# Kernel tuning notes

Measured on AMD Instinct MI355X. Metric: run time of the kernel, lower is better.

## Reference

```python
import jax, jax.numpy as jnp
import numpy as np

TEMP = 0.07
BATCH, DIM, NUM_ATTRS = 8192, 512, 4
NUM_PROTOS = 2 ** NUM_ATTRS  # all binary combos present => unique() size is static


def setup_inputs() -> dict:
    key = jax.random.key(0)
    z_flowed = jax.random.normal(key, (BATCH, DIM), dtype=jnp.float32)
    # binary attribute combos, all 16 present; first column = MSB (matches torch.unique row sort)
    combo = jnp.arange(BATCH, dtype=jnp.int32) % NUM_PROTOS
    shifts = jnp.arange(NUM_ATTRS - 1, -1, -1, dtype=jnp.int32)
    attributes = ((combo[:, None] >> shifts[None, :]) & 1).astype(jnp.float32)
    return {"z_flowed": z_flowed, "attributes": attributes}


def _l2norm(x, axis=-1, eps=1e-12):
    n = jnp.sqrt(jnp.sum(x * x, axis=axis, keepdims=True))
    return x / jnp.maximum(n, eps)  # F.normalize semantics


def reference(z_flowed, attributes):
    B, D = z_flowed.shape
    num_attrs = attributes.shape[1]
    P = 2 ** num_attrs
    z_norm = _l2norm(z_flowed, axis=1)

    # inverse indices of torch.unique(attributes, dim=0): binary row -> code (MSB = col 0)
    shifts = jnp.arange(num_attrs - 1, -1, -1)
    inverse = jnp.sum((attributes > 0.5).astype(jnp.int32) * (1 << shifts)[None, :], axis=1)

    # prototype = normalized segment-mean of z_norm per attribute combo (detached)
    sums = jax.ops.segment_sum(z_norm, inverse, num_segments=P)          # [P, D]
    counts = jax.ops.segment_sum(jnp.ones((B,), z_norm.dtype), inverse, num_segments=P)
    means = sums / jnp.maximum(counts, 1.0)[:, None]
    prototypes = jax.lax.stop_gradient(_l2norm(means, axis=1))
    prototypes = jnp.where(counts[:, None] > 0, prototypes, 0.0)

    # prototype contrastive term
    proto_sim = (z_norm @ prototypes.T) / TEMP                            # [B, P]
    exp_sim = jnp.exp(proto_sim)
    pos = exp_sim[jnp.arange(B), inverse]
    alls = jnp.maximum(jnp.sum(exp_sim, axis=1), 1e-8)
    loss = -jnp.mean(jnp.log(pos / alls + 1e-8))

    # pairwise term (positives only when BOTH attribute rows are all-ones)
    pairwise = (z_norm @ z_norm.T) / TEMP                                 # [B, B]
    attr_sim = attributes @ attributes.T
    pos_mask = (attr_sim == num_attrs).astype(z_norm.dtype)
    pos_mask = pos_mask * (1.0 - jnp.eye(B, dtype=z_norm.dtype))
    exp_pw = jnp.exp(pairwise)
    pos_sims = jnp.sum(exp_pw * pos_mask, axis=1)
    all_sims = jnp.sum(exp_pw, axis=1) - jnp.diagonal(exp_pw)
    valid = jnp.sum(pos_mask, axis=1) > 0
    per_row = -jnp.log(pos_sims / (all_sims + 1e-8) + 1e-8)
    n_valid = jnp.sum(valid.astype(z_norm.dtype))
    pairwise_loss = jnp.sum(jnp.where(valid, per_row, 0.0)) / jnp.maximum(n_valid, 1.0)
    loss = jnp.where(n_valid > 0, 0.7 * loss + 0.3 * pairwise_loss, loss)
    return loss
```

## Files before the change

kernel.cpp:

```cpp
#include <hip/hip_runtime.h>
#include <math.h>

#define NB 8192
#define ND 512
#define NPROTO 16
#define NBLK 256
#define TINV 14.285714285714286f
#define PW_BLOCKS 256
#define PL_BLOCKS 256

typedef short short8 __attribute__((ext_vector_type(8)));
typedef float float4v __attribute__((ext_vector_type(4)));

__device__ __forceinline__ unsigned short f2bf(float f) {
  unsigned u = __builtin_bit_cast(unsigned, f);
  unsigned r = (u + 0x7FFFu + ((u >> 16) & 1u)) >> 16;
  return (unsigned short)r;
}
__device__ __forceinline__ float bflo(unsigned u) {
  return __builtin_bit_cast(float, u << 16);
}
__device__ __forceinline__ float bfhi(unsigned u) {
  return __builtin_bit_cast(float, u & 0xFFFF0000u);
}

__global__ __launch_bounds__(512) void k_norm(
    const float* __restrict__ z, const float* __restrict__ attr,
    unsigned short* __restrict__ znb, float* __restrict__ partialSum,
    int* __restrict__ code)
{
  __shared__ float acc[NPROTO * ND];
  const int t = threadIdx.x, lane = t & 63, wid = t >> 6;
  for (int i = t; i < NPROTO * ND; i += 512) acc[i] = 0.f;
  __syncthreads();
  #pragma unroll
  for (int rr = 0; rr < 4; ++rr) {
    const int r = blockIdx.x * 32 + wid * 4 + rr;
    const float4* zr4 = (const float4*)(z + (size_t)r * ND);
    const float4 va = zr4[lane];
    const float4 vb = zr4[lane + 64];
    float v[8] = {va.x, va.y, va.z, va.w, vb.x, vb.y, vb.z, vb.w};
    float s = 0.f;
    #pragma unroll
    for (int k = 0; k < 8; ++k) s += v[k] * v[k];
    #pragma unroll
    for (int o = 32; o > 0; o >>= 1) s += __shfl_xor(s, o);
    const float inv = 1.f / fmaxf(sqrtf(s), 1e-12f);
    const float* a = attr + (size_t)r * 4;
    const int c = (a[0] > 0.5f ? 8 : 0) | (a[1] > 0.5f ? 4 : 0) |
                  (a[2] > 0.5f ? 2 : 0) | (a[3] > 0.5f ? 1 : 0);
    float* accRow = acc + c * ND;
    #pragma unroll
    for (int k = 0; k < 8; ++k) {
      const float zv = v[k] * inv;
      atomicAdd(&accRow[k * 64 + lane], zv);
      znb[(size_t)r * ND + k * 64 + lane] = f2bf(zv);
    }
    if (lane == 0) code[r] = c;
  }
  __syncthreads();
  for (int i = t; i < NPROTO * ND; i += 512) {
    const int p = i >> 9, d = i & 511;
    partialSum[(size_t)((p << 8) | blockIdx.x) * ND + d] = acc[i];
  }
}

__global__ __launch_bounds__(256) void k_reduce1(
    const float* __restrict__ partialSum, float* __restrict__ partial2)
{
  const int t = threadIdx.x;
  const int p = blockIdx.x >> 4, c = blockIdx.x & 15;
  const float* base = partialSum + (size_t)(p * NBLK + c * 16) * ND;
  float s0 = 0.f, s1 = 0.f;
  #pragma unroll
  for (int k = 0; k < 16; ++k) {
    s0 += base[k * ND + t];
    s1 += base[k * ND + t + 256];
  }
  partial2[(size_t)(p * 16 + c) * ND + t] = s0;
  partial2[(size_t)(p * 16 + c) * ND + t + 256] = s1;
}

__global__ __launch_bounds__(512) void k_protonorm(
    const float* __restrict__ partial2, const int* __restrict__ code,
    float* __restrict__ protos, int* __restrict__ validList,
    int* __restrict__ validCnt)
{
  __shared__ float red[8];
  __shared__ int lcnt;
  const int t = threadIdx.x, lane = t & 63, wid = t >> 6;
  const int p = blockIdx.x;
  if (t == 0) lcnt = 0;
  __syncthreads();
  const float* base = partial2 + (size_t)p * 16 * ND;
  float s = 0.f;
  #pragma unroll
  for (int c = 0; c < 16; ++c)
    s += base[c * ND + t];
  float cl = 0.f;
  for (int r = t; r < NB; r += 512) {
    const int match = (code[r] == p) ? 1 : 0;
    cl += (float)match;
    if (p == NPROTO - 1 && match) {
      const int slot = atomicAdd(&lcnt, 1);
      validList[slot] = r;
    }
  }
  #pragma unroll
  for (int o = 32; o > 0; o >>= 1) cl += __shfl_xor(cl, o);
  if (lane == 0) red[wid] = cl;
  __syncthreads();
  const float cTot = red[0]+red[1]+red[2]+red[3]+red[4]+red[5]+red[6]+red[7];
  __syncthreads();
  const float mean = s / fmaxf(cTot, 1.f);
  float sq = mean * mean;
  #pragma unroll
  for (int o = 32; o > 0; o >>= 1) sq += __shfl_xor(sq, o);
  if (lane == 0) red[wid] = sq;
  __syncthreads();
  const float sum = red[0]+red[1]+red[2]+red[3]+red[4]+red[5]+red[6]+red[7];
  const float scale = (cTot > 0.f) ? 1.f / fmaxf(sqrtf(sum), 1e-12f) : 0.f;
  protos[p * ND + t] = mean * scale;
  if (p == NPROTO - 1 && t == 0) validCnt[0] = lcnt;
}

#define PLD (ND + 4)
#define SMEM_BYTES 41472
__global__ __launch_bounds__(512) void k_main(
    const unsigned short* __restrict__ znb, const float* __restrict__ protos,
    const int* __restrict__ code, const int* __restrict__ validList,
    const int* __restrict__ validCnt,
    float* __restrict__ partialAll, float* __restrict__ partialPos,
    float* __restrict__ plPart)
{
  __shared__ __align__(16) char smem[SMEM_BYTES];
  __shared__ float red3[8];
  const int t = threadIdx.x, lane = t & 63, wid = t >> 6;
  const int bi = blockIdx.x;
  if (bi < PW_BLOCKS) {
    unsigned short* aT = (unsigned short*)smem;
    unsigned short* bT = aT + 64 * 64;
    int* rowIdx = (int*)(bT + 256 * 64);
    unsigned char* aoSh = (unsigned char*)(rowIdx + 64);
    const int wv = wid >> 2, ww = wid & 3;
    const int m = validCnt[0];
    const int nIT = (m + 63) >> 6;
    const int items = nIT * 32;
    const int grp = lane >> 4, cl = lane & 15;
    for (int wi = bi; wi < items; wi += PW_BLOCKS) {
      const int i0 = (wi >> 5) * 64;
      const int jt = wi & 31;
      const int jb = jt * 256;
      __syncthreads();
      if (t < 64) rowIdx[t] = (i0 + t < m) ? validList[i0 + t] : -1;
      if (t < 256) aoSh[t] = (code[jb + t] == NPROTO - 1) ? 1 : 0;
      float4v acc[2][4];
      #pragma unroll
      for (int mi = 0; mi < 2; ++mi)
        #pragma unroll
        for (int nj = 0; nj < 4; ++nj) acc[mi][nj] = (float4v)(0.f);
      for (int kc = 0; kc < 8; ++kc) {
        const int k0 = kc * 64;
        __syncthreads();
        {
          const int ia = t >> 3, kq = t & 7;
          const int ri = rowIdx[ia];
          const int srow = (ri < 0) ? 0 : ri;
          const uint4 v = *(const uint4*)(znb + (size_t)srow * ND + k0 + kq * 8);
          *(uint4*)((char*)aT + ia * 128 + ((kq * 16) ^ ((ia & 7) << 4))) = v;
        }
        #pragma unroll
        for (int h = 0; h < 4; ++h) {
          const int f = t + h * 512;
          const int j = f >> 3, kq = f & 7;
          const uint4 v = *(const uint4*)(znb + (size_t)(jb + j) * ND + k0 + kq * 8);
          *(uint4*)((char*)bT + j * 128 + ((kq * 16) ^ ((j & 7) << 4))) = v;
        }
        __syncthreads();
        #pragma unroll
        for (int ks = 0; ks < 2; ++ks) {
          const int kb = ks * 64 + grp * 16;
          short8 af[2], bf[4];
          #pragma unroll
          for (int mi = 0; mi < 2; ++mi) {
            const int rw = wv * 32 + mi * 16 + cl;
            af[mi] = *(const short8*)((char*)aT + rw * 128 + (kb ^ ((rw & 7) << 4)));
          }
          #pragma unroll
          for (int nj = 0; nj < 4; ++nj) {
            const int rw = ww * 64 + nj * 16 + cl;
            bf[nj] = *(const short8*)((char*)bT + rw * 128 + (kb ^ ((rw & 7) << 4)));
          }
          #pragma unroll
          for (int mi = 0; mi < 2; ++mi)
            #pragma unroll
            for (int nj = 0; nj < 4; ++nj)
              acc[mi][nj] = __builtin_amdgcn_mfma_f32_16x16x32_bf16(af[mi], bf[nj], acc[mi][nj], 0, 0, 0);
        }
      }
      #pragma unroll
      for (int mi = 0; mi < 2; ++mi) {
        float sA[4] = {0.f, 0.f, 0.f, 0.f}, sP[4] = {0.f, 0.f, 0.f, 0.f};
        int ri[4];
        #pragma unroll
        for (int q = 0; q < 4; ++q) ri[q] = rowIdx[wv * 32 + mi * 16 + grp * 4 + q];
        #pragma unroll
        for (int nj = 0; nj < 4; ++nj) {
          const int jl = ww * 64 + nj * 16 + cl;
          const int jg = jb + jl;
          const float ao = aoSh[jl] ? 1.f : 0.f;
          #pragma unroll
          for (int q = 0; q < 4; ++q) {
            float e = __expf(acc[mi][nj][q] * TINV);
            e = (jg == ri[q]) ? 0.f : e;
            sA[q] += e;
            sP[q] += e * ao;
          }
        }
        #pragma unroll
        for (int q = 0; q < 4; ++q) {
          #pragma unroll
          for (int o = 1; o < 16; o <<= 1) {
            sA[q] += __shfl_xor(sA[q], o);
            sP[q] += __shfl_xor(sP[q], o);
          }
        }
        if (cl == 0) {
          const int slot0 = i0 + wv * 32 + mi * 16 + grp * 4;
          const int jt2 = jt * 4 + ww;
          if (slot0 + 3 < m) {
            *(float4*)&partialAll[(size_t)jt2 * NB + slot0] =
                make_float4(sA[0], sA[1], sA[2], sA[3]);
            *(float4*)&partialPos[(size_t)jt2 * NB + slot0] =
                make_float4(sP[0], sP[1], sP[2], sP[3]);
          } else {
            #pragma unroll
            for (int q = 0; q < 4; ++q) {
              if (slot0 + q < m) {
                partialAll[(size_t)jt2 * NB + slot0 + q] = sA[q];
                partialPos[(size_t)jt2 * NB + slot0 + q] = sP[q];
              }
            }
          }
        }
      }
    }
  } else {
    float* pl = (float*)smem;
    const int pb = bi - PW_BLOCKS;
    for (int i = t; i < NPROTO * ND; i += 512)
      pl[(i >> 9) * PLD + (i & 511)] = protos[i];
    __syncthreads();
    const int p = lane & 15, grp = lane >> 4;
    float lacc = 0.f;
    #pragma unroll
    for (int rr = 0; rr < 4; ++rr) {
      const int r = pb * 32 + wid * 4 + rr;
      const uint4* zr = (const uint4*)(znb + (size_t)r * ND + grp * 128);
      const float* pbp = &pl[p * PLD + grp * 128];
      float s = 0.f;
      #pragma unroll
      for (int it = 0; it < 16; ++it) {
        const uint4 u = zr[it];
        const float4 p0 = *(const float4*)(pbp + it * 8);
        const float4 p1 = *(const float4*)(pbp + it * 8 + 4);
        s += bflo(u.x)*p0.x + bfhi(u.x)*p0.y + bflo(u.y)*p0.z + bfhi(u.y)*p0.w;
        s += bflo(u.z)*p1.x + bfhi(u.z)*p1.y + bflo(u.w)*p1.z + bfhi(u.w)*p1.w;
      }
      s += __shfl_xor(s, 16);
      s += __shfl_xor(s, 32);
      const float e = __expf(s * TINV);
      float alls = e;
      alls += __shfl_xor(alls, 1);
      alls += __shfl_xor(alls, 2);
      alls += __shfl_xor(alls, 4);
      alls += __shfl_xor(alls, 8);
      const int c = code[r];
      const float pos = __shfl(e, (lane & ~15) | c);
      if (lane == 0) lacc += -logf(pos / fmaxf(alls, 1e-8f) + 1e-8f);
    }
    if (lane == 0) red3[wid] = lacc;
    __syncthreads();
    if (t == 0)
      plPart[pb] = red3[0]+red3[1]+red3[2]+red3[3]+red3[4]+red3[5]+red3[6]+red3[7];
  }
}

__global__ __launch_bounds__(1024) void k_final(
    const float* __restrict__ partialAll, const float* __restrict__ partialPos,
    const float* __restrict__ plPart, const int* __restrict__ validCnt,
    float* __restrict__ out)
{
  __shared__ float shA[1024], shP[1024];
  __shared__ float red[16], red2[16];
  const int t = threadIdx.x, lane = t & 63, wid = t >> 6;
  const int m = validCnt[0];
  const int nvalid = (m >= 2) ? m : 0;
  const int slot = t & 511, half = t >> 9;
  float sa = 0.f, sp = 0.f;
  if (slot < nvalid) {
    const int k0 = half * 64;
    #pragma unroll 8
    for (int k = k0; k < k0 + 64; ++k) {
      sa += partialAll[(size_t)k * NB + slot];
      sp += partialPos[(size_t)k * NB + slot];
    }
  }
  shA[t] = sa; shP[t] = sp;
  __syncthreads();
  float s = 0.f;
  if (t < 512 && slot < nvalid) {
    const float A = shA[t] + shA[t + 512];
    const float P = shP[t] + shP[t + 512];
    s = -logf(P / (A + 1e-8f) + 1e-8f);
  }
  float pls = (t < PL_BLOCKS) ? plPart[t] : 0.f;
  #pragma unroll
  for (int o = 32; o > 0; o >>= 1) {
    s += __shfl_xor(s, o);
    pls += __shfl_xor(pls, o);
  }
  if (lane == 0) { red[wid] = s; red2[wid] = pls; }
  __syncthreads();
  if (t == 0) {
    float total = 0.f, plTot = 0.f;
    #pragma unroll
    for (int w = 0; w < 16; ++w) { total += red[w]; plTot += red2[w]; }
    const float proto = plTot / (float)NB;
    float loss = proto;
    if (nvalid > 0) loss = 0.7f * proto + 0.3f * (total / (float)nvalid);
    out[0] = loss;
  }
}

extern "C" void kernel_launch(void* const* d_in, const int* in_sizes, int n_in,
                              void* d_out, int out_size, void* d_ws, size_t ws_size,
                              hipStream_t stream) {
  const float* z = (const float*)d_in[0];
  const float* attr = (const float*)d_in[1];
  unsigned short* znb = (unsigned short*)d_ws;
  float* partialSum = (float*)(znb + (size_t)NB * ND);
  float* partialAll = partialSum;
  float* partialPos = partialSum + (size_t)128 * NB;
  char* w = (char*)(partialSum + (size_t)NBLK * NPROTO * ND);
  float* partial2 = (float*)w;      w += (size_t)NPROTO * 16 * ND * 4;
  int* validCnt = (int*)w;          w += 16;
  int* code = (int*)w;              w += NB * 4;
  int* validList = (int*)w;         w += NB * 4;
  float* protos = (float*)w;        w += NPROTO * ND * 4;
  float* plPart = (float*)w;        w += PL_BLOCKS * 4;
  k_norm<<<dim3(NBLK), dim3(512), 0, stream>>>(z, attr, znb, partialSum, code);
  k_reduce1<<<dim3(256), dim3(256), 0, stream>>>(partialSum, partial2);
  k_protonorm<<<dim3(NPROTO), dim3(512), 0, stream>>>(partial2, code, protos,
                                                      validList, validCnt);
  k_main<<<dim3(PW_BLOCKS + PL_BLOCKS), dim3(512), 0, stream>>>(
      znb, protos, code, validList, validCnt, partialAll, partialPos, plPart);
  k_final<<<dim3(1), dim3(1024), 0, stream>>>(partialAll, partialPos, plPart,
                                              validCnt, (float*)d_out);
}
```

Before: 68.45 us.

## Parallelize final reduction across blocks with last-block atomic completion

The final reduction of per-row pairwise partial sums now runs on 64 blocks instead of one. Each wave sums the 128 partials of one valid row via cross-lane shuffles. Each block writes a partial loss, and the last block to finish (found with an atomic counter reset in k_norm) combines the block results with the prototype-term partials. This spreads the reduction's memory reads across many CUs, at the cost of atomics, threadfences and a counter that must be reset on every call.

```diff
diff --git a/kernel.cpp b/kernel.cpp
--- a/kernel.cpp
+++ b/kernel.cpp
@@ -8,6 +8,7 @@
 #define TINV 14.285714285714286f
 #define PW_BLOCKS 256
 #define PL_BLOCKS 256
+#define FIN_BLOCKS 64
 
 typedef short short8 __attribute__((ext_vector_type(8)));
 typedef float float4v __attribute__((ext_vector_type(4)));
@@ -27,11 +28,12 @@
 __global__ __launch_bounds__(512) void k_norm(
     const float* __restrict__ z, const float* __restrict__ attr,
     unsigned short* __restrict__ znb, float* __restrict__ partialSum,
-    int* __restrict__ code)
+    int* __restrict__ code, unsigned* __restrict__ doneCnt)
 {
   __shared__ float acc[NPROTO * ND];
   const int t = threadIdx.x, lane = t & 63, wid = t >> 6;
   for (int i = t; i < NPROTO * ND; i += 512) acc[i] = 0.f;
+  if (blockIdx.x == 0 && t == 0) doneCnt[0] = 0u;
   __syncthreads();
   #pragma unroll
   for (int rr = 0; rr < 4; ++rr) {
@@ -286,34 +288,43 @@
   }
 }
 
-__global__ __launch_bounds__(1024) void k_final(
+__global__ __launch_bounds__(512) void k_final(
     const float* __restrict__ partialAll, const float* __restrict__ partialPos,
     const float* __restrict__ plPart, const int* __restrict__ validCnt,
+    float* __restrict__ blockLoss, unsigned* __restrict__ doneCnt,
     float* __restrict__ out)
 {
-  __shared__ float shA[1024], shP[1024];
-  __shared__ float red[16], red2[16];
+  __shared__ float red[8], red2[8];
+  __shared__ bool isLast;
   const int t = threadIdx.x, lane = t & 63, wid = t >> 6;
+  const int bi = blockIdx.x;
   const int m = validCnt[0];
   const int nvalid = (m >= 2) ? m : 0;
-  const int slot = t & 511, half = t >> 9;
-  float sa = 0.f, sp = 0.f;
-  if (slot < nvalid) {
-    const int k0 = half * 64;
-    #pragma unroll 8
-    for (int k = k0; k < k0 + 64; ++k) {
-      sa += partialAll[(size_t)k * NB + slot];
-      sp += partialPos[(size_t)k * NB + slot];
-    }
-  }
-  shA[t] = sa; shP[t] = sp;
-  __syncthreads();
-  float s = 0.f;
-  if (t < 512 && slot < nvalid) {
-    const float A = shA[t] + shA[t + 512];
-    const float P = shP[t] + shP[t + 512];
-    s = -logf(P / (A + 1e-8f) + 1e-8f);
-  }
+  float bl = 0.f;
+  for (int s = bi * 8 + wid; s < nvalid; s += FIN_BLOCKS * 8) {
+    float a = partialAll[(size_t)lane * NB + s] +
+              partialAll[(size_t)(lane + 64) * NB + s];
+    float p = partialPos[(size_t)lane * NB + s] +
+              partialPos[(size_t)(lane + 64) * NB + s];
+    #pragma unroll
+    for (int o = 32; o > 0; o >>= 1) {
+      a += __shfl_xor(a, o);
+      p += __shfl_xor(p, o);
+    }
+    if (lane == 0) bl += -logf(p / (a + 1e-8f) + 1e-8f);
+  }
+  if (lane == 0) red[wid] = bl;
+  __syncthreads();
+  if (t == 0) {
+    blockLoss[bi] = red[0]+red[1]+red[2]+red[3]+red[4]+red[5]+red[6]+red[7];
+    __threadfence();
+    const unsigned v = atomicAdd(doneCnt, 1u);
+    isLast = (v == (unsigned)(FIN_BLOCKS - 1));
+  }
+  __syncthreads();
+  if (!isLast) return;
+  __threadfence();
+  float s = (t < FIN_BLOCKS) ? atomicAdd(&blockLoss[t], 0.f) : 0.f;
   float pls = (t < PL_BLOCKS) ? plPart[t] : 0.f;
   #pragma unroll
   for (int o = 32; o > 0; o >>= 1) {
@@ -323,9 +334,8 @@
   if (lane == 0) { red[wid] = s; red2[wid] = pls; }
   __syncthreads();
   if (t == 0) {
-    float total = 0.f, plTot = 0.f;
-    #pragma unroll
-    for (int w = 0; w < 16; ++w) { total += red[w]; plTot += red2[w]; }
+    const float total = red[0]+red[1]+red[2]+red[3]+red[4]+red[5]+red[6]+red[7];
+    const float plTot = red2[0]+red2[1]+red2[2]+red2[3]+red2[4]+red2[5]+red2[6]+red2[7];
     const float proto = plTot / (float)NB;
     float loss = proto;
     if (nvalid > 0) loss = 0.7f * proto + 0.3f * (total / (float)nvalid);
@@ -349,12 +359,16 @@
   int* validList = (int*)w;         w += NB * 4;
   float* protos = (float*)w;        w += NPROTO * ND * 4;
   float* plPart = (float*)w;        w += PL_BLOCKS * 4;
-  k_norm<<<dim3(NBLK), dim3(512), 0, stream>>>(z, attr, znb, partialSum, code);
+  float* blockLoss = (float*)w;     w += FIN_BLOCKS * 4;
+  unsigned* doneCnt = (unsigned*)w; w += 16;
+  k_norm<<<dim3(NBLK), dim3(512), 0, stream>>>(z, attr, znb, partialSum, code,
+                                               doneCnt);
   k_reduce1<<<dim3(256), dim3(256), 0, stream>>>(partialSum, partial2);
   k_protonorm<<<dim3(NPROTO), dim3(512), 0, stream>>>(partial2, code, protos,
                                                       validList, validCnt);
   k_main<<<dim3(PW_BLOCKS + PL_BLOCKS), dim3(512), 0, stream>>>(
       znb, protos, code, validList, validCnt, partialAll, partialPos, plPart);
-  k_final<<<dim3(1), dim3(1024), 0, stream>>>(partialAll, partialPos, plPart,
-                                              validCnt, (float*)d_out);
-}
+  k_final<<<dim3(FIN_BLOCKS), dim3(512), 0, stream>>>(
+      partialAll, partialPos, plPart, validCnt, blockLoss, doneCnt,
+      (float*)d_out);
+}
```

After: 66.64 us (median of 2 runs). -2.6%, faster.
